# Kernel optimization log

Measured on AMD Instinct MI355X. Metric: run time of the kernel, lower is better.

Reference implementation:

```python
import jax, jax.numpy as jnp
import numpy as np
from jax import lax

B, C_IN, H, W = 32, 128, 64, 64
K, C_OUT, KS = 8, 128, 3
HID = C_IN * 4  # extend = 4
TEMPERATURE = 1.0
PAD = 1


def setup_inputs() -> dict:
    key = jax.random.key(0)
    ks = jax.random.split(key, 7)
    x = jax.random.normal(ks[0], (B, C_IN, H, W), jnp.float32)
    prompt_param = jax.random.uniform(ks[1], (1, K, HID), jnp.float32)
    w1 = jax.random.normal(ks[2], (HID, C_IN), jnp.float32) * 0.05
    b1 = jnp.zeros((HID,), jnp.float32)
    w2 = jax.random.normal(ks[3], (HID, HID), jnp.float32) * 0.05
    b2 = jnp.zeros((HID,), jnp.float32)
    kernels_weights = jax.random.normal(ks[4], (K, C_OUT, C_IN, KS, KS), jnp.float32) * 0.05
    kernels_bias = jax.random.normal(ks[5], (K, C_OUT), jnp.float32) * 0.05
    return {
        'x': x, 'prompt_param': prompt_param,
        'w1': w1, 'b1': b1, 'w2': w2, 'b2': b2,
        'kernels_weights': kernels_weights, 'kernels_bias': kernels_bias,
    }


def reference(x, prompt_param, w1, b1, w2, b2, kernels_weights, kernels_bias):
    # Attention: global avg pool -> MLP -> prompt dot -> softmax over kernels
    pooled = jnp.mean(x, axis=(2, 3))                       # (B, C_in)
    h = jax.nn.relu(pooled @ w1.T + b1)                     # (B, HID)
    s = h @ w2.T + b2                                       # (B, HID)
    scores = jnp.sum(s[:, None, :] * prompt_param, axis=-1)  # (B, K)
    alphas = jax.nn.softmax(scores / TEMPERATURE, axis=-1)   # (B, K)

    # Per-sample kernel aggregation
    agg_w = jnp.einsum('bk,koihw->boihw', alphas, kernels_weights)  # (B,O,I,kh,kw)
    agg_b = alphas @ kernels_bias                                    # (B, O)

    # Per-sample conv2d (equivalent to the groups=B grouped-conv trick)
    def conv_one(xi, wi):
        # xi: (C_in,H,W), wi: (O,C_in,kh,kw)
        return lax.conv_general_dilated(
            xi[None], wi, window_strides=(1, 1),
            padding=((PAD, PAD), (PAD, PAD)),
            dimension_numbers=('NCHW', 'OIHW', 'NCHW'))[0]
    out = jax.vmap(conv_one)(x, agg_w)                       # (B,O,H,W)
    out = out + agg_b[:, :, None, None]
    return out
```

## Files before the change

kernel.cpp:

```cpp
#include <hip/hip_runtime.h>
#include <hip/hip_bf16.h>
#include <stdint.h>


typedef __bf16 v8bf __attribute__((ext_vector_type(8)));
typedef float  v4f  __attribute__((ext_vector_type(4)));

#define XT_OFF     0u
#define XT_BYTES   (32u*4096u*128u*2u)
#define AGGW_OFF   (XT_OFF + XT_BYTES)
#define AGGW_BYTES (32u*9u*128u*128u*2u)
#define PART_OFF   (AGGW_OFF)
#define PP_OFF     (AGGW_OFF + 0x100000u)
#define PB_OFF     (AGGW_OFF + 0x110000u)
#define ALPHA_OFF  (AGGW_OFF + AGGW_BYTES)
#define ALPHA_BYTES (32u*8u*4u)
#define AGGB_OFF   (ALPHA_OFF + ALPHA_BYTES)
#define AGGB_BYTES (32u*128u*4u)

typedef const void __attribute__((address_space(1))) gconst_t;
typedef void       __attribute__((address_space(3))) ldsv_t;

__device__ __forceinline__ void g2l16(const void* g, void* l) {
  __builtin_amdgcn_global_load_lds((gconst_t*)g, (ldsv_t*)l, 16, 0, 0);
}

#define VM_WAIT(N)  asm volatile("s_waitcnt vmcnt(" #N ")" ::: "memory")
#define LGKM_WAIT0() asm volatile("s_waitcnt lgkmcnt(0)" ::: "memory")
#define SCHED_FENCE() __builtin_amdgcn_sched_barrier(0)
#define RAW_BARRIER() __builtin_amdgcn_s_barrier()

__global__ __launch_bounds__(512) void prompt_pre_kernel(
    const float* __restrict__ prompt, const float* __restrict__ w2,
    const float* __restrict__ b2, float* __restrict__ pp,
    float* __restrict__ pb) {
  const int k = blockIdx.x, i = threadIdx.x;
  __shared__ float sP[512];
  sP[i] = prompt[k * 512 + i];
  __syncthreads();
  float acc = 0.0f;
  #pragma unroll 8
  for (int j = 0; j < 512; ++j) acc = fmaf(sP[j], w2[j * 512 + i], acc);
  pp[k * 512 + i] = acc;
  if (i == 0) {
    float a = 0.0f;
    for (int j = 0; j < 512; ++j) a = fmaf(sP[j], b2[j], a);
    pb[k] = a;
  }
}

__global__ __launch_bounds__(256) void pool_convert_kernel(
    const float* __restrict__ x, float* __restrict__ partial,
    __hip_bfloat16* __restrict__ xT) {
  const int b = blockIdx.x >> 6;
  const int h = blockIdx.x & 63;
  const int tid = threadIdx.x;
  const int wv = tid >> 6, lane = tid & 63;
  const int wq = lane & 15;
  const int cl = lane >> 4;
  __shared__ __align__(16) __hip_bfloat16 sT[64 * 130];

  const float* xrow = x + (((size_t)b * 128) << 12) + (h << 6);
  #pragma unroll
  for (int i = 0; i < 8; ++i) {
    int c = wv * 32 + i * 4 + cl;
    float4 v = *(const float4*)&xrow[((size_t)c << 12) + wq * 4];
    int w0 = wq * 4;
    sT[(w0 + 0) * 130 + c] = __float2bfloat16(v.x);
    sT[(w0 + 1) * 130 + c] = __float2bfloat16(v.y);
    sT[(w0 + 2) * 130 + c] = __float2bfloat16(v.z);
    sT[(w0 + 3) * 130 + c] = __float2bfloat16(v.w);
    float s = v.x + v.y + v.z + v.w;
    s += __shfl_xor(s, 1);
    s += __shfl_xor(s, 2);
    s += __shfl_xor(s, 4);
    s += __shfl_xor(s, 8);
    if (wq == 0) partial[((b << 6) + h) * 128 + c] = s;
  }
  __syncthreads();
  const int pw = tid >> 2;
  const int piece = tid & 3;
  const uint32_t* s32 = (const uint32_t*)sT;
  uint32_t vals[16];
  #pragma unroll
  for (int j = 0; j < 16; ++j) vals[j] = s32[pw * 65 + piece * 16 + j];
  char* dst = (char*)xT + ((((size_t)b << 6) + h) * 64 + pw) * 256 + piece * 64;
  #pragma unroll
  for (int j = 0; j < 4; ++j)
    ((uint4*)dst)[j] = make_uint4(vals[4*j], vals[4*j+1], vals[4*j+2], vals[4*j+3]);
}

__global__ __launch_bounds__(256) void attn_fused_kernel(
    const float* __restrict__ partial, const float* __restrict__ w1,
    const float* __restrict__ b1, const float* __restrict__ pp,
    const float* __restrict__ pb, const float* __restrict__ kbias,
    float* __restrict__ alphas, float* __restrict__ aggb) {
  const int b = blockIdx.x, tid = threadIdx.x;
  __shared__ float sTmp[256];
  __shared__ float sPool[128];
  __shared__ float sH[512];
  __shared__ float sS[8], sA[8];

  {
    const int c = tid & 127, hh = tid >> 7;
    const float* src = partial + ((size_t)b << 6) * 128 + hh * 128 + c;
    float acc = 0.0f;
    #pragma unroll
    for (int h2 = 0; h2 < 32; ++h2) acc += src[h2 * 256];
    sTmp[tid] = acc;
  }
  __syncthreads();
  if (tid < 128) sPool[tid] = (sTmp[tid] + sTmp[tid + 128]) * (1.0f / 4096.0f);
  __syncthreads();

  #pragma unroll
  for (int q = 0; q < 2; ++q) {
    const int j = q * 256 + tid;
    const float* wr = w1 + j * 128;
    float acc = 0.0f;
    #pragma unroll
    for (int i4 = 0; i4 < 32; ++i4) {
      float4 wv = *(const float4*)&wr[i4 * 4];
      acc += wv.x * sPool[i4*4] + wv.y * sPool[i4*4+1] +
             wv.z * sPool[i4*4+2] + wv.w * sPool[i4*4+3];
    }
    sH[j] = fmaxf(acc + b1[j], 0.0f);
  }
  __syncthreads();

  {
    const int k = tid >> 5, seg = tid & 31;
    const float* ppk = pp + k * 512 + seg * 16;
    const float* hk  = sH + seg * 16;
    float acc = 0.0f;
    #pragma unroll
    for (int t4 = 0; t4 < 4; ++t4) {
      float4 pv = *(const float4*)&ppk[t4 * 4];
      acc += pv.x * hk[t4*4] + pv.y * hk[t4*4+1] +
             pv.z * hk[t4*4+2] + pv.w * hk[t4*4+3];
    }
    #pragma unroll
    for (int m = 16; m > 0; m >>= 1) acc += __shfl_xor(acc, m);
    if (seg == 0) sS[k] = acc + pb[k];
  }
  __syncthreads();

  if (tid == 0) {
    float mx = sS[0];
    for (int k = 1; k < 8; ++k) mx = fmaxf(mx, sS[k]);
    float sum = 0.0f, e[8];
    for (int k = 0; k < 8; ++k) { e[k] = expf(sS[k] - mx); sum += e[k]; }
    float inv = 1.0f / sum;
    for (int k = 0; k < 8; ++k) sA[k] = e[k] * inv;
  }
  __syncthreads();
  if (tid < 8) alphas[b * 8 + tid] = sA[tid];
  if (tid < 128) {
    float acc = 0.0f;
    #pragma unroll
    for (int k = 0; k < 8; ++k) acc = fmaf(sA[k], kbias[k * 128 + tid], acc);
    aggb[b * 128 + tid] = acc;
  }
}

__global__ __launch_bounds__(128) void agg_weights_kernel(
    const float* __restrict__ kw, const float* __restrict__ alphas,
    __hip_bfloat16* __restrict__ aggw) {
  const int co = blockIdx.x;
  const int bg = blockIdx.y;
  const int tid = threadIdx.x;
  __shared__ float sA[64];
  __shared__ float sbuf[1152];
  if (tid < 64) sA[tid] = alphas[bg * 64 + tid];
  __syncthreads();

  float acc[8][9];
  #pragma unroll
  for (int bb = 0; bb < 8; ++bb)
    #pragma unroll
    for (int q = 0; q < 9; ++q) acc[bb][q] = 0.0f;

  for (int k = 0; k < 8; ++k) {
    const float* src = kw + ((size_t)(k * 128 + co)) * 1152;
    float v[9];
    #pragma unroll
    for (int q = 0; q < 9; ++q) v[q] = src[tid + 128 * q];
    #pragma unroll
    for (int bb = 0; bb < 8; ++bb) {
      float a = sA[bb * 8 + k];
      #pragma unroll
      for (int q = 0; q < 9; ++q) acc[bb][q] = fmaf(a, v[q], acc[bb][q]);
    }
  }

  #pragma unroll 1
  for (int bb = 0; bb < 8; ++bb) {
    __syncthreads();
    #pragma unroll
    for (int q = 0; q < 9; ++q) sbuf[tid + 128 * q] = acc[bb][q];
    __syncthreads();
    const int b = bg * 8 + bb;
    #pragma unroll
    for (int t = 0; t < 9; ++t)
      aggw[(((size_t)(b * 9 + t) * 128 + co) << 7) + tid] =
          __float2bfloat16(sbuf[tid * 9 + t]);
  }
}

#define XTILE_B 33792
#define ABUF_B  16384

__global__ __launch_bounds__(256) void dyn_conv_kernel(
    const __hip_bfloat16* __restrict__ xT, const __hip_bfloat16* __restrict__ aggw,
    const float* __restrict__ aggb, float* __restrict__ out) {
  const int tile = blockIdx.x;
  const int b    = blockIdx.y;
  const int tid  = threadIdx.x;
  const int wv = tid >> 6, lane = tid & 63;
  const int wm = wv >> 1, wn = wv & 1;
  const int lm = lane & 15, quad = lane >> 4;
  const int r0 = tile * 2;

  __shared__ __align__(16) char smem[XTILE_B + 2 * ABUF_B + 512];
  char* xb = smem;
  char* abuf = smem + XTILE_B;
  float* sBias = (float*)(smem + XTILE_B + 2 * ABUF_B);

  if (tid < 128) sBias[tid] = aggb[b * 128 + tid];

  for (int pos = tid; pos < 264; pos += 256) {
    int tr = pos / 66, tc = pos - tr * 66;
    int h = r0 - 1 + tr, w = tc - 1;
    if ((unsigned)h >= 64u || (unsigned)w >= 64u) {
      int4* d = (int4*)(xb + pos * 128);
      #pragma unroll
      for (int i = 0; i < 8; ++i) d[i] = make_int4(0, 0, 0, 0);
    }
  }

  const char* xTb = (const char*)xT + ((size_t)b << 20);
  const char* awb = (const char*)aggw + (size_t)b * 294912;

  auto stageX = [&](int half) {
    for (int i = wv; i < 33; i += 4) {
      int P = (i << 6) + lane;
      int pos = P >> 3, slot = P & 7;
      int tr = pos / 66, tc = pos - tr * 66;
      int h = r0 - 1 + tr, w = tc - 1;
      char* dst = xb + (i << 10);
      if ((unsigned)h < 64u && (unsigned)w < 64u) {
        int p = slot ^ (pos & 7);
        const char* src = xTb + (((h << 6) + w) << 8) + (half << 7) + (p << 4);
        g2l16(src, dst);
      }
    }
  };

  auto stageA = [&](int tap, int half) {
    char* ab = abuf + (tap & 1) * ABUF_B;
    #pragma unroll
    for (int sub = 0; sub < 2; ++sub) {
      const int cic = half * 2 + sub;
      const char* base = awb + (tap << 15) + (cic << 6);
      #pragma unroll
      for (int jj = 0; jj < 2; ++jj) {
        int j = wv * 2 + jj;
        int co = (j << 4) + (lane >> 2);
        int f = lane & 3;
        int p = f ^ ((co >> 1) & 3);
        g2l16(base + (co << 8) + (p << 4), ab + sub * 8192 + (j << 10));
      }
    }
  };

  int posb[4];
  #pragma unroll
  for (int ni = 0; ni < 4; ++ni) {
    int n = wn * 64 + ni * 16 + lm;
    posb[ni] = (n >> 6) * 66 + (n & 63);
  }
  const int fA = (quad ^ ((lm >> 1) & 3)) << 4;
  int aoff[4];
  #pragma unroll
  for (int mi = 0; mi < 4; ++mi) {
    int co = wm * 64 + mi * 16 + lm;
    aoff[mi] = (co << 6) + fA;
  }

  v4f acc[4][4];
  #pragma unroll
  for (int mi = 0; mi < 4; ++mi)
    #pragma unroll
    for (int ni = 0; ni < 4; ++ni) acc[mi][ni] = v4f{0.f, 0.f, 0.f, 0.f};

  auto computeTap = [&](int tap) {
    const int th = tap / 3, tw = tap - th * 3;
    const int tapAdd = th * 66 + tw;
    char* ab = abuf + (tap & 1) * ABUF_B;
    #pragma unroll
    for (int sub = 0; sub < 2; ++sub) {
      v8bf af[4], bfr[4];
      #pragma unroll
      for (int mi = 0; mi < 4; ++mi)
        af[mi] = *(const v8bf*)(ab + sub * 8192 + aoff[mi]);
      const int piece = (sub << 2) | quad;
      #pragma unroll
      for (int ni = 0; ni < 4; ++ni) {
        int pos = posb[ni] + tapAdd;
        int pp = (piece ^ (pos & 7)) << 4;
        bfr[ni] = *(const v8bf*)(xb + (pos << 7) + pp);
      }
      #pragma unroll
      for (int mi = 0; mi < 4; ++mi)
        #pragma unroll
        for (int ni = 0; ni < 4; ++ni)
          acc[mi][ni] = __builtin_amdgcn_mfma_f32_16x16x32_bf16(
              af[mi], bfr[ni], acc[mi][ni], 0, 0, 0);
    }
  };

  #define TAP_STEP(t, half)                                            \
    computeTap(t);                                                     \
    if ((t) < 8) {                                                     \
      LGKM_WAIT0(); SCHED_FENCE();                                     \
      RAW_BARRIER(); SCHED_FENCE();                                    \
      if ((t) + 2 < 9) { stageA((t) + 2, half); VM_WAIT(4); }          \
      else             { VM_WAIT(0); }                                 \
      SCHED_FENCE();                                                   \
      RAW_BARRIER(); SCHED_FENCE();                                    \
    }

  stageA(0, 0);
  stageA(1, 0);
  stageX(0);
  __syncthreads();
  TAP_STEP(0, 0) TAP_STEP(1, 0) TAP_STEP(2, 0) TAP_STEP(3, 0) TAP_STEP(4, 0)
  TAP_STEP(5, 0) TAP_STEP(6, 0) TAP_STEP(7, 0) TAP_STEP(8, 0)
  LGKM_WAIT0(); SCHED_FENCE();
  __syncthreads();
  stageX(1);
  stageA(0, 1);
  stageA(1, 1);
  __syncthreads();
  TAP_STEP(0, 1) TAP_STEP(1, 1) TAP_STEP(2, 1) TAP_STEP(3, 1) TAP_STEP(4, 1)
  TAP_STEP(5, 1) TAP_STEP(6, 1) TAP_STEP(7, 1) TAP_STEP(8, 1)
  #undef TAP_STEP

  #pragma unroll
  for (int mi = 0; mi < 4; ++mi) {
    #pragma unroll
    for (int r = 0; r < 4; ++r) {
      int co = wm * 64 + mi * 16 + quad * 4 + r;
      float bias = sBias[co];
      #pragma unroll
      for (int ni = 0; ni < 4; ++ni) {
        int n = wn * 64 + ni * 16 + lm;
        out[(((size_t)(b * 128 + co)) << 12) + tile * 128 + n] =
            acc[mi][ni][r] + bias;
      }
    }
  }
}

extern "C" void kernel_launch(void* const* d_in, const int* in_sizes, int n_in,
                              void* d_out, int out_size, void* d_ws, size_t ws_size,
                              hipStream_t stream) {
  const float* x      = (const float*)d_in[0];
  const float* prompt = (const float*)d_in[1];
  const float* w1     = (const float*)d_in[2];
  const float* b1     = (const float*)d_in[3];
  const float* w2     = (const float*)d_in[4];
  const float* b2     = (const float*)d_in[5];
  const float* kw     = (const float*)d_in[6];
  const float* kb     = (const float*)d_in[7];
  float* out = (float*)d_out;
  char* ws = (char*)d_ws;

  __hip_bfloat16* xT   = (__hip_bfloat16*)(ws + XT_OFF);
  __hip_bfloat16* aggw = (__hip_bfloat16*)(ws + AGGW_OFF);
  float* part   = (float*)(ws + PART_OFF);
  float* pp     = (float*)(ws + PP_OFF);
  float* pb     = (float*)(ws + PB_OFF);
  float* alphas = (float*)(ws + ALPHA_OFF);
  float* aggb   = (float*)(ws + AGGB_OFF);

  prompt_pre_kernel<<<8, 512, 0, stream>>>(prompt, w2, b2, pp, pb);
  pool_convert_kernel<<<2048, 256, 0, stream>>>(x, part, xT);
  attn_fused_kernel<<<32, 256, 0, stream>>>(part, w1, b1, pp, pb, kb,
                                            alphas, aggb);
  agg_weights_kernel<<<dim3(128, 4), 128, 0, stream>>>(kw, alphas, aggw);
  dyn_conv_kernel<<<dim3(32, 32), 256, 0, stream>>>(xT, aggw, aggb, out);
}
```

Before: 246.2 us.

## Enlarge conv tile to four rows and parallelize prompt precompute over splits

Measured after the change: 214.4 us. -12.9%, faster.

```diff
diff --git a/kernel.cpp b/kernel.cpp
--- a/kernel.cpp
+++ b/kernel.cpp
@@ -12,7 +12,7 @@
 #define AGGW_BYTES (32u*9u*128u*128u*2u)
 #define PART_OFF   (AGGW_OFF)
 #define PP_OFF     (AGGW_OFF + 0x100000u)
-#define PB_OFF     (AGGW_OFF + 0x110000u)
+#define PBP_OFF    (AGGW_OFF + 0x120000u)
 #define ALPHA_OFF  (AGGW_OFF + AGGW_BYTES)
 #define ALPHA_BYTES (32u*8u*4u)
 #define AGGB_OFF   (ALPHA_OFF + ALPHA_BYTES)
@@ -25,27 +25,25 @@
   __builtin_amdgcn_global_load_lds((gconst_t*)g, (ldsv_t*)l, 16, 0, 0);
 }
 
-#define VM_WAIT(N)  asm volatile("s_waitcnt vmcnt(" #N ")" ::: "memory")
-#define LGKM_WAIT0() asm volatile("s_waitcnt lgkmcnt(0)" ::: "memory")
-#define SCHED_FENCE() __builtin_amdgcn_sched_barrier(0)
-#define RAW_BARRIER() __builtin_amdgcn_s_barrier()
-
 __global__ __launch_bounds__(512) void prompt_pre_kernel(
     const float* __restrict__ prompt, const float* __restrict__ w2,
     const float* __restrict__ b2, float* __restrict__ pp,
-    float* __restrict__ pb) {
-  const int k = blockIdx.x, i = threadIdx.x;
-  __shared__ float sP[512];
-  sP[i] = prompt[k * 512 + i];
+    float* __restrict__ pbp) {
+  const int k = blockIdx.x, js = blockIdx.y;
+  const int i = threadIdx.x;
+  __shared__ float sP[64];
+  if (i < 64) sP[i] = prompt[k * 512 + js * 64 + i];
   __syncthreads();
   float acc = 0.0f;
+  const float* wcol = w2 + (js * 64) * 512 + i;
   #pragma unroll 8
-  for (int j = 0; j < 512; ++j) acc = fmaf(sP[j], w2[j * 512 + i], acc);
-  pp[k * 512 + i] = acc;
-  if (i == 0) {
-    float a = 0.0f;
-    for (int j = 0; j < 512; ++j) a = fmaf(sP[j], b2[j], a);
-    pb[k] = a;
+  for (int jj = 0; jj < 64; ++jj) acc = fmaf(sP[jj], wcol[jj * 512], acc);
+  pp[(k * 8 + js) * 512 + i] = acc;
+  if (i < 64) {
+    float v = sP[i] * b2[js * 64 + i];
+    #pragma unroll
+    for (int m = 32; m > 0; m >>= 1) v += __shfl_xor(v, m);
+    if (i == 0) pbp[k * 8 + js] = v;
   }
 }
 
@@ -93,7 +91,7 @@
 __global__ __launch_bounds__(256) void attn_fused_kernel(
     const float* __restrict__ partial, const float* __restrict__ w1,
     const float* __restrict__ b1, const float* __restrict__ pp,
-    const float* __restrict__ pb, const float* __restrict__ kbias,
+    const float* __restrict__ pbp, const float* __restrict__ kbias,
     float* __restrict__ alphas, float* __restrict__ aggb) {
   const int b = blockIdx.x, tid = threadIdx.x;
   __shared__ float sTmp[256];
@@ -130,18 +128,26 @@
 
   {
     const int k = tid >> 5, seg = tid & 31;
-    const float* ppk = pp + k * 512 + seg * 16;
-    const float* hk  = sH + seg * 16;
+    const float* hk = sH + seg * 16;
     float acc = 0.0f;
     #pragma unroll
-    for (int t4 = 0; t4 < 4; ++t4) {
-      float4 pv = *(const float4*)&ppk[t4 * 4];
-      acc += pv.x * hk[t4*4] + pv.y * hk[t4*4+1] +
-             pv.z * hk[t4*4+2] + pv.w * hk[t4*4+3];
+    for (int js = 0; js < 8; ++js) {
+      const float* ppk = pp + (k * 8 + js) * 512 + seg * 16;
+      #pragma unroll
+      for (int t4 = 0; t4 < 4; ++t4) {
+        float4 pv = *(const float4*)&ppk[t4 * 4];
+        acc += pv.x * hk[t4*4] + pv.y * hk[t4*4+1] +
+               pv.z * hk[t4*4+2] + pv.w * hk[t4*4+3];
+      }
     }
     #pragma unroll
     for (int m = 16; m > 0; m >>= 1) acc += __shfl_xor(acc, m);
-    if (seg == 0) sS[k] = acc + pb[k];
+    if (seg == 0) {
+      float pbk = 0.0f;
+      #pragma unroll
+      for (int js = 0; js < 8; ++js) pbk += pbp[k * 8 + js];
+      sS[k] = acc + pbk;
+    }
   }
   __syncthreads();
 
@@ -207,10 +213,10 @@
   }
 }
 
-#define XTILE_B 33792
-#define ABUF_B  16384
-
-__global__ __launch_bounds__(256) void dyn_conv_kernel(
+#define XTILE_B 50688
+#define ABUF_B  8192
+
+__global__ __launch_bounds__(256, 1) void dyn_conv_kernel(
     const __hip_bfloat16* __restrict__ xT, const __hip_bfloat16* __restrict__ aggw,
     const float* __restrict__ aggb, float* __restrict__ out) {
   const int tile = blockIdx.x;
@@ -219,7 +225,7 @@
   const int wv = tid >> 6, lane = tid & 63;
   const int wm = wv >> 1, wn = wv & 1;
   const int lm = lane & 15, quad = lane >> 4;
-  const int r0 = tile * 2;
+  const int r0 = tile * 4;
 
   __shared__ __align__(16) char smem[XTILE_B + 2 * ABUF_B + 512];
   char* xb = smem;
@@ -228,7 +234,7 @@
 
   if (tid < 128) sBias[tid] = aggb[b * 128 + tid];
 
-  for (int pos = tid; pos < 264; pos += 256) {
+  for (int pos = tid; pos < 396; pos += 256) {
     int tr = pos / 66, tc = pos - tr * 66;
     int h = r0 - 1 + tr, w = tc - 1;
     if ((unsigned)h >= 64u || (unsigned)w >= 64u) {
@@ -242,13 +248,13 @@
   const char* awb = (const char*)aggw + (size_t)b * 294912;
 
   auto stageX = [&](int half) {
-    for (int i = wv; i < 33; i += 4) {
+    for (int i = wv; i < 50; i += 4) {
       int P = (i << 6) + lane;
       int pos = P >> 3, slot = P & 7;
       int tr = pos / 66, tc = pos - tr * 66;
       int h = r0 - 1 + tr, w = tc - 1;
       char* dst = xb + (i << 10);
-      if ((unsigned)h < 64u && (unsigned)w < 64u) {
+      if (pos < 396 && (unsigned)h < 64u && (unsigned)w < 64u) {
         int p = slot ^ (pos & 7);
         const char* src = xTb + (((h << 6) + w) << 8) + (half << 7) + (p << 4);
         g2l16(src, dst);
@@ -256,27 +262,25 @@
     }
   };
 
-  auto stageA = [&](int tap, int half) {
-    char* ab = abuf + (tap & 1) * ABUF_B;
-    #pragma unroll
-    for (int sub = 0; sub < 2; ++sub) {
-      const int cic = half * 2 + sub;
-      const char* base = awb + (tap << 15) + (cic << 6);
-      #pragma unroll
-      for (int jj = 0; jj < 2; ++jj) {
-        int j = wv * 2 + jj;
-        int co = (j << 4) + (lane >> 2);
-        int f = lane & 3;
-        int p = f ^ ((co >> 1) & 3);
-        g2l16(base + (co << 8) + (p << 4), ab + sub * 8192 + (j << 10));
-      }
+  auto stageA = [&](int c, int half) {
+    const int tap = c >> 1, sub = c & 1;
+    const int cic = half * 2 + sub;
+    char* ab = abuf + (c & 1) * ABUF_B;
+    const char* base = awb + (tap << 15) + (cic << 6);
+    #pragma unroll
+    for (int jj = 0; jj < 2; ++jj) {
+      int j = wv * 2 + jj;
+      int co = (j << 4) + (lane >> 2);
+      int f = lane & 3;
+      int p = f ^ ((co >> 1) & 3);
+      g2l16(base + (co << 8) + (p << 4), ab + (j << 10));
     }
   };
 
-  int posb[4];
-  #pragma unroll
-  for (int ni = 0; ni < 4; ++ni) {
-    int n = wn * 64 + ni * 16 + lm;
+  int posb[8];
+  #pragma unroll
+  for (int ni = 0; ni < 8; ++ni) {
+    int n = wn * 128 + ni * 16 + lm;
     posb[ni] = (n >> 6) * 66 + (n & 63);
   }
   const int fA = (quad ^ ((lm >> 1) & 3)) << 4;
@@ -287,64 +291,61 @@
     aoff[mi] = (co << 6) + fA;
   }
 
-  v4f acc[4][4];
+  v4f acc[4][8];
   #pragma unroll
   for (int mi = 0; mi < 4; ++mi)
     #pragma unroll
-    for (int ni = 0; ni < 4; ++ni) acc[mi][ni] = v4f{0.f, 0.f, 0.f, 0.f};
-
-  auto computeTap = [&](int tap) {
+    for (int ni = 0; ni < 8; ++ni) acc[mi][ni] = v4f{0.f, 0.f, 0.f, 0.f};
+
+  auto computeChunk = [&](int c) {
+    const int tap = c >> 1, sub = c & 1;
     const int th = tap / 3, tw = tap - th * 3;
     const int tapAdd = th * 66 + tw;
-    char* ab = abuf + (tap & 1) * ABUF_B;
-    #pragma unroll
-    for (int sub = 0; sub < 2; ++sub) {
-      v8bf af[4], bfr[4];
-      #pragma unroll
-      for (int mi = 0; mi < 4; ++mi)
-        af[mi] = *(const v8bf*)(ab + sub * 8192 + aoff[mi]);
-      const int piece = (sub << 2) | quad;
-      #pragma unroll
-      for (int ni = 0; ni < 4; ++ni) {
-        int pos = posb[ni] + tapAdd;
-        int pp = (piece ^ (pos & 7)) << 4;
-        bfr[ni] = *(const v8bf*)(xb + (pos << 7) + pp);
+    char* ab = abuf + (c & 1) * ABUF_B;
+    v8bf af[4];
+    #pragma unroll
+    for (int mi = 0; mi < 4; ++mi) af[mi] = *(const v8bf*)(ab + aoff[mi]);
+    const int piece = (sub << 2) | quad;
+    #pragma unroll
+    for (int g = 0; g < 2; ++g) {
+      v8bf bfr[4];
+      #pragma unroll
+      for (int nj = 0; nj < 4; ++nj) {
+        int pos = posb[g * 4 + nj] + tapAdd;
+        int pq = (piece ^ (pos & 7)) << 4;
+        bfr[nj] = *(const v8bf*)(xb + (pos << 7) + pq);
       }
       #pragma unroll
       for (int mi = 0; mi < 4; ++mi)
         #pragma unroll
-        for (int ni = 0; ni < 4; ++ni)
-          acc[mi][ni] = __builtin_amdgcn_mfma_f32_16x16x32_bf16(
-              af[mi], bfr[ni], acc[mi][ni], 0, 0, 0);
+        for (int nj = 0; nj < 4; ++nj)
+          acc[mi][g * 4 + nj] = __builtin_amdgcn_mfma_f32_16x16x32_bf16(
+              af[mi], bfr[nj], acc[mi][g * 4 + nj], 0, 0, 0);
     }
   };
-
-  #define TAP_STEP(t, half)                                            \
-    computeTap(t);                                                     \
-    if ((t) < 8) {                                                     \
-      LGKM_WAIT0(); SCHED_FENCE();                                     \
-      RAW_BARRIER(); SCHED_FENCE();                                    \
-      if ((t) + 2 < 9) { stageA((t) + 2, half); VM_WAIT(4); }          \
-      else             { VM_WAIT(0); }                                 \
-      SCHED_FENCE();                                                   \
-      RAW_BARRIER(); SCHED_FENCE();                                    \
-    }
 
   stageA(0, 0);
   stageA(1, 0);
   stageX(0);
   __syncthreads();
-  TAP_STEP(0, 0) TAP_STEP(1, 0) TAP_STEP(2, 0) TAP_STEP(3, 0) TAP_STEP(4, 0)
-  TAP_STEP(5, 0) TAP_STEP(6, 0) TAP_STEP(7, 0) TAP_STEP(8, 0)
-  LGKM_WAIT0(); SCHED_FENCE();
-  __syncthreads();
+  #pragma unroll
+  for (int c = 0; c < 18; ++c) {
+    computeChunk(c);
+    __syncthreads();
+    if (c + 2 < 18) stageA(c + 2, 0);
+  }
   stageX(1);
   stageA(0, 1);
   stageA(1, 1);
   __syncthreads();
-  TAP_STEP(0, 1) TAP_STEP(1, 1) TAP_STEP(2, 1) TAP_STEP(3, 1) TAP_STEP(4, 1)
-  TAP_STEP(5, 1) TAP_STEP(6, 1) TAP_STEP(7, 1) TAP_STEP(8, 1)
-  #undef TAP_STEP
+  #pragma unroll
+  for (int c = 0; c < 18; ++c) {
+    computeChunk(c);
+    if (c < 17) {
+      __syncthreads();
+      if (c + 2 < 18) stageA(c + 2, 1);
+    }
+  }
 
   #pragma unroll
   for (int mi = 0; mi < 4; ++mi) {
@@ -353,9 +354,9 @@
       int co = wm * 64 + mi * 16 + quad * 4 + r;
       float bias = sBias[co];
       #pragma unroll
-      for (int ni = 0; ni < 4; ++ni) {
-        int n = wn * 64 + ni * 16 + lm;
-        out[(((size_t)(b * 128 + co)) << 12) + tile * 128 + n] =
+      for (int ni = 0; ni < 8; ++ni) {
+        int n = wn * 128 + ni * 16 + lm;
+        out[(((size_t)(b * 128 + co)) << 12) + tile * 256 + n] =
             acc[mi][ni][r] + bias;
       }
     }
@@ -380,14 +381,14 @@
   __hip_bfloat16* aggw = (__hip_bfloat16*)(ws + AGGW_OFF);
   float* part   = (float*)(ws + PART_OFF);
   float* pp     = (float*)(ws + PP_OFF);
-  float* pb     = (float*)(ws + PB_OFF);
+  float* pbp    = (float*)(ws + PBP_OFF);
   float* alphas = (float*)(ws + ALPHA_OFF);
   float* aggb   = (float*)(ws + AGGB_OFF);
 
-  prompt_pre_kernel<<<8, 512, 0, stream>>>(prompt, w2, b2, pp, pb);
+  prompt_pre_kernel<<<dim3(8, 8), 512, 0, stream>>>(prompt, w2, b2, pp, pbp);
   pool_convert_kernel<<<2048, 256, 0, stream>>>(x, part, xT);
-  attn_fused_kernel<<<32, 256, 0, stream>>>(part, w1, b1, pp, pb, kb,
+  attn_fused_kernel<<<32, 256, 0, stream>>>(part, w1, b1, pp, pbp, kb,
                                             alphas, aggb);
   agg_weights_kernel<<<dim3(128, 4), 128, 0, stream>>>(kw, alphas, aggw);
-  dyn_conv_kernel<<<dim3(32, 32), 256, 0, stream>>>(xT, aggw, aggb, out);
-}
+  dyn_conv_kernel<<<dim3(16, 32), 256, 0, stream>>>(xT, aggw, aggb, out);
+}
```
